# Kernel tuning notes

Measured on AMD Instinct MI355X. Metric: run time of the kernel, lower is better.

Reference implementation:

```python
import jax, jax.numpy as jnp
import numpy as np

NUM_HEADS = 8


def _conv1(x, w, b):
    # 1x1x1 Conv3d == per-voxel channel linear map. x: [B,C,D,H,W], w: [O,C], b: [O]
    return jnp.einsum('bcdhw,oc->bodhw', x, w) + b[None, :, None, None, None]


def setup_inputs() -> dict:
    key = jax.random.key(0)
    ks = jax.random.split(key, 7)
    B, C, D, H, W = 1, 64, 16, 16, 16
    s = 0.02
    return {
        'decoder_features': jax.random.normal(ks[0], (B, C, D, H, W), jnp.float32),
        'mae_features': jax.random.normal(ks[1], (B, C, D, H, W), jnp.float32),
        'q_w': jax.random.normal(ks[2], (C, C), jnp.float32) * s,
        'q_b': jnp.zeros((C,), jnp.float32),
        'k_w': jax.random.normal(ks[3], (C, C), jnp.float32) * s,
        'k_b': jnp.zeros((C,), jnp.float32),
        'v_w': jax.random.normal(ks[4], (C, C), jnp.float32) * s,
        'v_b': jnp.zeros((C,), jnp.float32),
        'o_w': jax.random.normal(ks[5], (C, C), jnp.float32) * s,
        'o_b': jnp.zeros((C,), jnp.float32),
    }


def reference(decoder_features, mae_features, q_w, q_b, k_w, k_b, v_w, v_b, o_w, o_b):
    B, C, D, H, W = decoder_features.shape
    nh = NUM_HEADS
    hd = C // nh
    N = D * H * W
    scale = hd ** -0.5

    def split_heads(x):
        # [B,C,D,H,W] -> [B, nh, N, hd]
        return x.reshape(B, nh, hd, N).transpose(0, 1, 3, 2)

    Q = split_heads(_conv1(decoder_features, q_w, q_b))
    K = split_heads(_conv1(mae_features, k_w, k_b))
    V = split_heads(_conv1(mae_features, v_w, v_b))

    attn = jax.nn.softmax(jnp.einsum('bhnc,bhmc->bhnm', Q, K) * scale, axis=-1)
    out = jnp.einsum('bhnm,bhmc->bhnc', attn, V)  # [B, nh, N, hd]
    out = out.transpose(0, 1, 3, 2).reshape(B, C, D, H, W)
    return _conv1(out, o_w, o_b)
```

## Files before the change

kernel.cpp:

```cpp
#include <hip/hip_runtime.h>
#include <hip/hip_bf16.h>
#include <math.h>


#define N_VOX 4096
#define NH 8
#define KS 8
#define KPS (N_VOX / KS)
#define QSCALE 0.51010813f

typedef unsigned short ushort_t;
typedef __attribute__((ext_vector_type(8))) short bf16x8;
typedef __attribute__((ext_vector_type(16))) float f32x16;

__device__ __forceinline__ unsigned short f2bf(float f) {
  union { float f; unsigned u; } v; v.f = f;
  unsigned r = v.u + 0x7FFFu + ((v.u >> 16) & 1u);
  return (unsigned short)(r >> 16);
}
__device__ __forceinline__ unsigned pk2bf(float a, float b) {
  __hip_bfloat162 h = __float22bfloat162_rn(float2{a, b});
  union { __hip_bfloat162 h; unsigned u; } c; c.h = h;
  return c.u;
}
__device__ __forceinline__ float ex2(float x) { return __builtin_amdgcn_exp2f(x); }

__global__ __launch_bounds__(256) void qkv_pack(
    const float* __restrict__ dec, const float* __restrict__ mae,
    const float* __restrict__ qw, const float* __restrict__ qb_,
    const float* __restrict__ kw, const float* __restrict__ kb,
    const float* __restrict__ vw, const float* __restrict__ vb,
    ushort_t* __restrict__ Qp, ushort_t* __restrict__ KpZ,
    ushort_t* __restrict__ VtP) {
  const int bx = blockIdx.x;
  const int n = blockIdx.y * 256 + threadIdx.x;

  if (bx < 8) {
    const int h = bx;
    float x[64];
#pragma unroll
    for (int c = 0; c < 64; ++c) x[c] = dec[c * N_VOX + n];
    float qv[8];
#pragma unroll
    for (int j = 0; j < 8; ++j) {
      const int o = h * 8 + j;
      float a = qb_[o];
#pragma unroll
      for (int c = 0; c < 64; ++c) a = fmaf(x[c], qw[o * 64 + c], a);
      qv[j] = a * QSCALE;
    }
    uint4 pk;
    pk.x = pk2bf(qv[0], qv[1]); pk.y = pk2bf(qv[2], qv[3]);
    pk.z = pk2bf(qv[4], qv[5]); pk.w = pk2bf(qv[6], qv[7]);
    *(uint4*)(Qp + ((size_t)h * N_VOX + n) * 8) = pk;
  } else {
    const int h = bx - 8;
    float x[64];
#pragma unroll
    for (int c = 0; c < 64; ++c) x[c] = mae[c * N_VOX + n];
    float kv[8], vv[8];
#pragma unroll
    for (int j = 0; j < 8; ++j) {
      const int o = h * 8 + j;
      float a = kb[o], v = vb[o];
#pragma unroll
      for (int c = 0; c < 64; ++c) {
        a = fmaf(x[c], kw[o * 64 + c], a);
        v = fmaf(x[c], vw[o * 64 + c], v);
      }
      kv[j] = a; vv[j] = v;
    }
    uint4 pk;
    pk.x = pk2bf(kv[0], kv[1]); pk.y = pk2bf(kv[2], kv[3]);
    pk.z = pk2bf(kv[4], kv[5]); pk.w = pk2bf(kv[6], kv[7]);
    ushort_t* krow = KpZ + ((size_t)h * N_VOX + n) * 16;
    *(uint4*)(krow) = pk;
    *(uint4*)(krow + 8) = make_uint4(0, 0, 0, 0);

    const size_t base =
        (((size_t)h * (N_VOX / 16) + (n >> 4)) * 64 + ((n >> 3) & 1) * 32) * 8 +
        (n & 7);
#pragma unroll
    for (int d = 0; d < 8; ++d) VtP[base + (size_t)d * 8] = f2bf(vv[d]);
    VtP[base + 8 * 8] = 0x3F80;
  }
}

__global__ __launch_bounds__(256, 4) void attn_mfma(
    const ushort_t* __restrict__ Qp, const ushort_t* __restrict__ KpZ,
    const ushort_t* __restrict__ VtP, float* __restrict__ o_part) {
  const int tid = threadIdx.x;
  const int lane = tid & 63;
  const int wave = tid >> 6;
  const int l31 = lane & 31;
  const int lhalf = lane >> 5;
  const int h = blockIdx.y;
  const int ks = blockIdx.z;
  const int qb = blockIdx.x * 256 + wave * 64;

  __shared__ ushort_t P_lds[8][32 * 36];

  bf16x8 qfrag0 = *(const bf16x8*)(Qp + ((size_t)h * N_VOX + qb + l31) * 8);
  bf16x8 qfrag1 = *(const bf16x8*)(Qp + ((size_t)h * N_VOX + qb + 32 + l31) * 8);

  f32x16 zf, acc0, acc1;
#pragma unroll
  for (int i = 0; i < 16; ++i) { zf[i] = 0.f; acc0[i] = 0.f; acc1[i] = 0.f; }

  const ushort_t* KpH = KpZ + (size_t)h * N_VOX * 16 + lhalf * 8;
  const ushort_t* VtPH = VtP + (size_t)h * (N_VOX / 16) * 64 * 8;
  ushort_t* pb0 = &P_lds[wave * 2 + 0][l31 * 36];
  ushort_t* pb1 = &P_lds[wave * 2 + 1][l31 * 36];
  const int kbeg = ks * KPS;

#pragma unroll 1
  for (int kk = 0; kk < KPS; kk += 32) {
    const int kcur = kbeg + kk;
    bf16x8 kf = *(const bf16x8*)(KpH + (size_t)(kcur + l31) * 16);
    bf16x8 vf0 = *(const bf16x8*)(VtPH + ((size_t)((kcur >> 4) + 0) * 64 + lane) * 8);
    bf16x8 vf1 = *(const bf16x8*)(VtPH + ((size_t)((kcur >> 4) + 1) * 64 + lane) * 8);

    f32x16 s0 = __builtin_amdgcn_mfma_f32_32x32x16_bf16(kf, qfrag0, zf, 0, 0, 0);
    f32x16 s1 = __builtin_amdgcn_mfma_f32_32x32x16_bf16(kf, qfrag1, zf, 0, 0, 0);

#pragma unroll
    for (int G = 0; G < 4; ++G) {
      uint2 w;
      w.x = pk2bf(ex2(s0[G * 4 + 0]), ex2(s0[G * 4 + 1]));
      w.y = pk2bf(ex2(s0[G * 4 + 2]), ex2(s0[G * 4 + 3]));
      *(uint2*)(pb0 + G * 8 + lhalf * 4) = w;
    }
#pragma unroll
    for (int G = 0; G < 4; ++G) {
      uint2 w;
      w.x = pk2bf(ex2(s1[G * 4 + 0]), ex2(s1[G * 4 + 1]));
      w.y = pk2bf(ex2(s1[G * 4 + 2]), ex2(s1[G * 4 + 3]));
      *(uint2*)(pb1 + G * 8 + lhalf * 4) = w;
    }

#pragma unroll
    for (int grp = 0; grp < 2; ++grp) {
      union { bf16x8 v; uint2 u[2]; } p0, p1;
      p0.u[0] = *(const uint2*)(pb0 + grp * 16 + lhalf * 8);
      p0.u[1] = *(const uint2*)(pb0 + grp * 16 + lhalf * 8 + 4);
      p1.u[0] = *(const uint2*)(pb1 + grp * 16 + lhalf * 8);
      p1.u[1] = *(const uint2*)(pb1 + grp * 16 + lhalf * 8 + 4);
      const bf16x8 vf = grp ? vf1 : vf0;
      acc0 = __builtin_amdgcn_mfma_f32_32x32x16_bf16(p0.v, vf, acc0, 0, 0, 0);
      acc1 = __builtin_amdgcn_mfma_f32_32x32x16_bf16(p1.v, vf, acc1, 0, 0, 0);
    }
  }

  if (l31 < 9) {
    float* ob = o_part + ((size_t)(ks * NH + h) * 9 + l31) * N_VOX;
#pragma unroll
    for (int t = 0; t < 2; ++t) {
      const f32x16 a = t ? acc1 : acc0;
      const int qst = qb + t * 32 + 4 * lhalf;
#pragma unroll
      for (int G = 0; G < 4; ++G) {
        float4 v4 = make_float4(a[G * 4 + 0], a[G * 4 + 1], a[G * 4 + 2], a[G * 4 + 3]);
        *(float4*)(ob + qst + 8 * G) = v4;
      }
    }
  }
}

__global__ __launch_bounds__(256) void combine_proj(
    const float* __restrict__ o_part, const float* __restrict__ ow,
    const float* __restrict__ obias, float* __restrict__ out) {
  const int og = blockIdx.x;
  const int n = blockIdx.y * 256 + threadIdx.x;

  float rinv[NH];
#pragma unroll
  for (int h = 0; h < NH; ++h) {
    float l = 0.f;
#pragma unroll
    for (int s = 0; s < KS; ++s)
      l += o_part[((size_t)(s * NH + h) * 9 + 8) * N_VOX + n];
    rinv[h] = 1.0f / l;
  }

  float acc[8];
#pragma unroll
  for (int j = 0; j < 8; ++j) acc[j] = obias[og * 8 + j];

#pragma unroll 2
  for (int c = 0; c < 64; ++c) {
    const int h = c >> 3, d = c & 7;
    float so = 0.f;
#pragma unroll
    for (int s = 0; s < KS; ++s)
      so += o_part[((size_t)(s * NH + h) * 9 + d) * N_VOX + n];
    const float x = so * rinv[h];
#pragma unroll
    for (int j = 0; j < 8; ++j)
      acc[j] = fmaf(x, ow[(og * 8 + j) * 64 + c], acc[j]);
  }
#pragma unroll
  for (int j = 0; j < 8; ++j) out[(size_t)(og * 8 + j) * N_VOX + n] = acc[j];
}

extern "C" void kernel_launch(void* const* d_in, const int* in_sizes, int n_in,
                              void* d_out, int out_size, void* d_ws, size_t ws_size,
                              hipStream_t stream) {
  const float* dec = (const float*)d_in[0];
  const float* mae = (const float*)d_in[1];
  const float* qw = (const float*)d_in[2];
  const float* qb = (const float*)d_in[3];
  const float* kw = (const float*)d_in[4];
  const float* kb = (const float*)d_in[5];
  const float* vw = (const float*)d_in[6];
  const float* vb = (const float*)d_in[7];
  const float* ow = (const float*)d_in[8];
  const float* ob = (const float*)d_in[9];
  float* out = (float*)d_out;
  char* ws = (char*)d_ws;

  const size_t OFF_QP = 0;
  const size_t OFF_KP = 0x80000;
  const size_t OFF_VT = 0x180000;
  const size_t OFF_OPART = 0x380000;

  ushort_t* Qp = (ushort_t*)(ws + OFF_QP);
  ushort_t* KpZ = (ushort_t*)(ws + OFF_KP);
  ushort_t* VtP = (ushort_t*)(ws + OFF_VT);
  float* o_part = (float*)(ws + OFF_OPART);

  qkv_pack<<<dim3(16, 16), 256, 0, stream>>>(dec, mae, qw, qb, kw, kb, vw, vb,
                                             Qp, KpZ, VtP);
  attn_mfma<<<dim3(16, 8, KS), 256, 0, stream>>>(Qp, KpZ, VtP, o_part);
  combine_proj<<<dim3(8, 16), 256, 0, stream>>>(o_part, ow, ob, out);
}
```

Before: 154.9 us.

## Fuse QKV, attention, and projection into one persistent kernel with grid barriers

Replaces the three kernel launches with a single 1024-block kernel that runs the QKV projection, split-K attention, and combine/output projection as phases separated by a software grid barrier built on atomics. The goal is to remove launch overhead and the gaps between kernels. The combine phase is reworked to give each block 4 output channels instead of 8 across 256 blocks. The barrier needs all 1024 blocks resident at once, which means 4 blocks per CU of 256 threads; if occupancy falls short it deadlocks. It also adds a memset launch and idles blocks during the light phases.

Result: slower. 376.6 us (+143.1%).

```diff
diff --git a/kernel.cpp b/kernel.cpp
--- a/kernel.cpp
+++ b/kernel.cpp
@@ -7,6 +7,7 @@
 #define NH 8
 #define KS 8
 #define KPS (N_VOX / KS)
+#define NBLK 1024
 #define QSCALE 0.51010813f
 
 typedef unsigned short ushort_t;
@@ -25,181 +26,208 @@
 }
 __device__ __forceinline__ float ex2(float x) { return __builtin_amdgcn_exp2f(x); }
 
-__global__ __launch_bounds__(256) void qkv_pack(
+__device__ __forceinline__ void grid_barrier(unsigned* cnt, unsigned* gen,
+                                             int tid) {
+  __syncthreads();
+  if (tid == 0) {
+    __threadfence();
+    unsigned g = atomicAdd(gen, 0u);
+    unsigned v = atomicAdd(cnt, 1u);
+    if (v == NBLK - 1) {
+      atomicExch(cnt, 0u);
+      __threadfence();
+      atomicAdd(gen, 1u);
+    } else {
+      while (atomicAdd(gen, 0u) == g) __builtin_amdgcn_s_sleep(4);
+    }
+    __threadfence();
+  }
+  __syncthreads();
+}
+
+__global__ __launch_bounds__(256, 4) void fused_xattn(
     const float* __restrict__ dec, const float* __restrict__ mae,
     const float* __restrict__ qw, const float* __restrict__ qb_,
     const float* __restrict__ kw, const float* __restrict__ kb,
     const float* __restrict__ vw, const float* __restrict__ vb,
+    const float* __restrict__ ow, const float* __restrict__ obias,
     ushort_t* __restrict__ Qp, ushort_t* __restrict__ KpZ,
-    ushort_t* __restrict__ VtP) {
-  const int bx = blockIdx.x;
-  const int n = blockIdx.y * 256 + threadIdx.x;
-
-  if (bx < 8) {
-    const int h = bx;
-    float x[64];
-#pragma unroll
-    for (int c = 0; c < 64; ++c) x[c] = dec[c * N_VOX + n];
-    float qv[8];
-#pragma unroll
-    for (int j = 0; j < 8; ++j) {
-      const int o = h * 8 + j;
-      float a = qb_[o];
-#pragma unroll
-      for (int c = 0; c < 64; ++c) a = fmaf(x[c], qw[o * 64 + c], a);
-      qv[j] = a * QSCALE;
-    }
-    uint4 pk;
-    pk.x = pk2bf(qv[0], qv[1]); pk.y = pk2bf(qv[2], qv[3]);
-    pk.z = pk2bf(qv[4], qv[5]); pk.w = pk2bf(qv[6], qv[7]);
-    *(uint4*)(Qp + ((size_t)h * N_VOX + n) * 8) = pk;
-  } else {
-    const int h = bx - 8;
-    float x[64];
-#pragma unroll
-    for (int c = 0; c < 64; ++c) x[c] = mae[c * N_VOX + n];
-    float kv[8], vv[8];
-#pragma unroll
-    for (int j = 0; j < 8; ++j) {
-      const int o = h * 8 + j;
-      float a = kb[o], v = vb[o];
-#pragma unroll
-      for (int c = 0; c < 64; ++c) {
-        a = fmaf(x[c], kw[o * 64 + c], a);
-        v = fmaf(x[c], vw[o * 64 + c], v);
-      }
-      kv[j] = a; vv[j] = v;
-    }
-    uint4 pk;
-    pk.x = pk2bf(kv[0], kv[1]); pk.y = pk2bf(kv[2], kv[3]);
-    pk.z = pk2bf(kv[4], kv[5]); pk.w = pk2bf(kv[6], kv[7]);
-    ushort_t* krow = KpZ + ((size_t)h * N_VOX + n) * 16;
-    *(uint4*)(krow) = pk;
-    *(uint4*)(krow + 8) = make_uint4(0, 0, 0, 0);
-
-    const size_t base =
-        (((size_t)h * (N_VOX / 16) + (n >> 4)) * 64 + ((n >> 3) & 1) * 32) * 8 +
-        (n & 7);
-#pragma unroll
-    for (int d = 0; d < 8; ++d) VtP[base + (size_t)d * 8] = f2bf(vv[d]);
-    VtP[base + 8 * 8] = 0x3F80;
-  }
-}
-
-__global__ __launch_bounds__(256, 4) void attn_mfma(
-    const ushort_t* __restrict__ Qp, const ushort_t* __restrict__ KpZ,
-    const ushort_t* __restrict__ VtP, float* __restrict__ o_part) {
+    ushort_t* __restrict__ VtP, float* __restrict__ o_part,
+    unsigned* __restrict__ bar, float* __restrict__ out) {
+  const int b = blockIdx.x;
   const int tid = threadIdx.x;
-  const int lane = tid & 63;
-  const int wave = tid >> 6;
-  const int l31 = lane & 31;
-  const int lhalf = lane >> 5;
-  const int h = blockIdx.y;
-  const int ks = blockIdx.z;
-  const int qb = blockIdx.x * 256 + wave * 64;
+  unsigned* cnt = bar;
+  unsigned* gen = bar + 1;
 
   __shared__ ushort_t P_lds[8][32 * 36];
 
-  bf16x8 qfrag0 = *(const bf16x8*)(Qp + ((size_t)h * N_VOX + qb + l31) * 8);
-  bf16x8 qfrag1 = *(const bf16x8*)(Qp + ((size_t)h * N_VOX + qb + 32 + l31) * 8);
-
-  f32x16 zf, acc0, acc1;
-#pragma unroll
-  for (int i = 0; i < 16; ++i) { zf[i] = 0.f; acc0[i] = 0.f; acc1[i] = 0.f; }
-
-  const ushort_t* KpH = KpZ + (size_t)h * N_VOX * 16 + lhalf * 8;
-  const ushort_t* VtPH = VtP + (size_t)h * (N_VOX / 16) * 64 * 8;
-  ushort_t* pb0 = &P_lds[wave * 2 + 0][l31 * 36];
-  ushort_t* pb1 = &P_lds[wave * 2 + 1][l31 * 36];
-  const int kbeg = ks * KPS;
+  if (b < 256) {
+    const int bx = b >> 4;
+    const int n = (b & 15) * 256 + tid;
+    if (bx < 8) {
+      const int h = bx;
+      float x[64];
+#pragma unroll
+      for (int c = 0; c < 64; ++c) x[c] = dec[c * N_VOX + n];
+      float qv[8];
+#pragma unroll
+      for (int j = 0; j < 8; ++j) {
+        const int o = h * 8 + j;
+        float a = qb_[o];
+#pragma unroll
+        for (int c = 0; c < 64; ++c) a = fmaf(x[c], qw[o * 64 + c], a);
+        qv[j] = a * QSCALE;
+      }
+      uint4 pk;
+      pk.x = pk2bf(qv[0], qv[1]); pk.y = pk2bf(qv[2], qv[3]);
+      pk.z = pk2bf(qv[4], qv[5]); pk.w = pk2bf(qv[6], qv[7]);
+      *(uint4*)(Qp + ((size_t)h * N_VOX + n) * 8) = pk;
+    } else {
+      const int h = bx - 8;
+      float x[64];
+#pragma unroll
+      for (int c = 0; c < 64; ++c) x[c] = mae[c * N_VOX + n];
+      float kv[8], vv[8];
+#pragma unroll
+      for (int j = 0; j < 8; ++j) {
+        const int o = h * 8 + j;
+        float a = kb[o], v = vb[o];
+#pragma unroll
+        for (int c = 0; c < 64; ++c) {
+          a = fmaf(x[c], kw[o * 64 + c], a);
+          v = fmaf(x[c], vw[o * 64 + c], v);
+        }
+        kv[j] = a; vv[j] = v;
+      }
+      uint4 pk;
+      pk.x = pk2bf(kv[0], kv[1]); pk.y = pk2bf(kv[2], kv[3]);
+      pk.z = pk2bf(kv[4], kv[5]); pk.w = pk2bf(kv[6], kv[7]);
+      ushort_t* krow = KpZ + ((size_t)h * N_VOX + n) * 16;
+      *(uint4*)(krow) = pk;
+      *(uint4*)(krow + 8) = make_uint4(0, 0, 0, 0);
+
+      const size_t base =
+          (((size_t)h * (N_VOX / 16) + (n >> 4)) * 64 + ((n >> 3) & 1) * 32) * 8 +
+          (n & 7);
+#pragma unroll
+      for (int d = 0; d < 8; ++d) VtP[base + (size_t)d * 8] = f2bf(vv[d]);
+      VtP[base + 8 * 8] = 0x3F80;
+    }
+  }
+
+  grid_barrier(cnt, gen, tid);
+
+  {
+    const int lane = tid & 63;
+    const int wave = tid >> 6;
+    const int l31 = lane & 31;
+    const int lhalf = lane >> 5;
+    const int qt = b & 15;
+    const int h = (b >> 4) & 7;
+    const int ks = b >> 7;
+    const int qb = qt * 256 + wave * 64;
+
+    bf16x8 qfrag0 = *(const bf16x8*)(Qp + ((size_t)h * N_VOX + qb + l31) * 8);
+    bf16x8 qfrag1 = *(const bf16x8*)(Qp + ((size_t)h * N_VOX + qb + 32 + l31) * 8);
+
+    f32x16 zf, acc0, acc1;
+#pragma unroll
+    for (int i = 0; i < 16; ++i) { zf[i] = 0.f; acc0[i] = 0.f; acc1[i] = 0.f; }
+
+    const ushort_t* KpH = KpZ + (size_t)h * N_VOX * 16 + lhalf * 8;
+    const ushort_t* VtPH = VtP + (size_t)h * (N_VOX / 16) * 64 * 8;
+    ushort_t* pb0 = &P_lds[wave * 2 + 0][l31 * 36];
+    ushort_t* pb1 = &P_lds[wave * 2 + 1][l31 * 36];
+    const int kbeg = ks * KPS;
 
 #pragma unroll 1
-  for (int kk = 0; kk < KPS; kk += 32) {
-    const int kcur = kbeg + kk;
-    bf16x8 kf = *(const bf16x8*)(KpH + (size_t)(kcur + l31) * 16);
-    bf16x8 vf0 = *(const bf16x8*)(VtPH + ((size_t)((kcur >> 4) + 0) * 64 + lane) * 8);
-    bf16x8 vf1 = *(const bf16x8*)(VtPH + ((size_t)((kcur >> 4) + 1) * 64 + lane) * 8);
-
-    f32x16 s0 = __builtin_amdgcn_mfma_f32_32x32x16_bf16(kf, qfrag0, zf, 0, 0, 0);
-    f32x16 s1 = __builtin_amdgcn_mfma_f32_32x32x16_bf16(kf, qfrag1, zf, 0, 0, 0);
-
-#pragma unroll
-    for (int G = 0; G < 4; ++G) {
-      uint2 w;
-      w.x = pk2bf(ex2(s0[G * 4 + 0]), ex2(s0[G * 4 + 1]));
-      w.y = pk2bf(ex2(s0[G * 4 + 2]), ex2(s0[G * 4 + 3]));
-      *(uint2*)(pb0 + G * 8 + lhalf * 4) = w;
-    }
-#pragma unroll
-    for (int G = 0; G < 4; ++G) {
-      uint2 w;
-      w.x = pk2bf(ex2(s1[G * 4 + 0]), ex2(s1[G * 4 + 1]));
-      w.y = pk2bf(ex2(s1[G * 4 + 2]), ex2(s1[G * 4 + 3]));
-      *(uint2*)(pb1 + G * 8 + lhalf * 4) = w;
-    }
-
-#pragma unroll
-    for (int grp = 0; grp < 2; ++grp) {
-      union { bf16x8 v; uint2 u[2]; } p0, p1;
-      p0.u[0] = *(const uint2*)(pb0 + grp * 16 + lhalf * 8);
-      p0.u[1] = *(const uint2*)(pb0 + grp * 16 + lhalf * 8 + 4);
-      p1.u[0] = *(const uint2*)(pb1 + grp * 16 + lhalf * 8);
-      p1.u[1] = *(const uint2*)(pb1 + grp * 16 + lhalf * 8 + 4);
-      const bf16x8 vf = grp ? vf1 : vf0;
-      acc0 = __builtin_amdgcn_mfma_f32_32x32x16_bf16(p0.v, vf, acc0, 0, 0, 0);
-      acc1 = __builtin_amdgcn_mfma_f32_32x32x16_bf16(p1.v, vf, acc1, 0, 0, 0);
-    }
-  }
-
-  if (l31 < 9) {
-    float* ob = o_part + ((size_t)(ks * NH + h) * 9 + l31) * N_VOX;
-#pragma unroll
-    for (int t = 0; t < 2; ++t) {
-      const f32x16 a = t ? acc1 : acc0;
-      const int qst = qb + t * 32 + 4 * lhalf;
+    for (int kk = 0; kk < KPS; kk += 32) {
+      const int kcur = kbeg + kk;
+      bf16x8 kf = *(const bf16x8*)(KpH + (size_t)(kcur + l31) * 16);
+      bf16x8 vf0 = *(const bf16x8*)(VtPH + ((size_t)((kcur >> 4) + 0) * 64 + lane) * 8);
+      bf16x8 vf1 = *(const bf16x8*)(VtPH + ((size_t)((kcur >> 4) + 1) * 64 + lane) * 8);
+
+      f32x16 s0 = __builtin_amdgcn_mfma_f32_32x32x16_bf16(kf, qfrag0, zf, 0, 0, 0);
+      f32x16 s1 = __builtin_amdgcn_mfma_f32_32x32x16_bf16(kf, qfrag1, zf, 0, 0, 0);
+
 #pragma unroll
       for (int G = 0; G < 4; ++G) {
-        float4 v4 = make_float4(a[G * 4 + 0], a[G * 4 + 1], a[G * 4 + 2], a[G * 4 + 3]);
-        *(float4*)(ob + qst + 8 * G) = v4;
-      }
-    }
-  }
-}
-
-__global__ __launch_bounds__(256) void combine_proj(
-    const float* __restrict__ o_part, const float* __restrict__ ow,
-    const float* __restrict__ obias, float* __restrict__ out) {
-  const int og = blockIdx.x;
-  const int n = blockIdx.y * 256 + threadIdx.x;
-
-  float rinv[NH];
-#pragma unroll
-  for (int h = 0; h < NH; ++h) {
-    float l = 0.f;
-#pragma unroll
-    for (int s = 0; s < KS; ++s)
-      l += o_part[((size_t)(s * NH + h) * 9 + 8) * N_VOX + n];
-    rinv[h] = 1.0f / l;
-  }
-
-  float acc[8];
-#pragma unroll
-  for (int j = 0; j < 8; ++j) acc[j] = obias[og * 8 + j];
+        uint2 w;
+        w.x = pk2bf(ex2(s0[G * 4 + 0]), ex2(s0[G * 4 + 1]));
+        w.y = pk2bf(ex2(s0[G * 4 + 2]), ex2(s0[G * 4 + 3]));
+        *(uint2*)(pb0 + G * 8 + lhalf * 4) = w;
+      }
+#pragma unroll
+      for (int G = 0; G < 4; ++G) {
+        uint2 w;
+        w.x = pk2bf(ex2(s1[G * 4 + 0]), ex2(s1[G * 4 + 1]));
+        w.y = pk2bf(ex2(s1[G * 4 + 2]), ex2(s1[G * 4 + 3]));
+        *(uint2*)(pb1 + G * 8 + lhalf * 4) = w;
+      }
+
+#pragma unroll
+      for (int grp = 0; grp < 2; ++grp) {
+        union { bf16x8 v; uint2 u[2]; } p0, p1;
+        p0.u[0] = *(const uint2*)(pb0 + grp * 16 + lhalf * 8);
+        p0.u[1] = *(const uint2*)(pb0 + grp * 16 + lhalf * 8 + 4);
+        p1.u[0] = *(const uint2*)(pb1 + grp * 16 + lhalf * 8);
+        p1.u[1] = *(const uint2*)(pb1 + grp * 16 + lhalf * 8 + 4);
+        const bf16x8 vf = grp ? vf1 : vf0;
+        acc0 = __builtin_amdgcn_mfma_f32_32x32x16_bf16(p0.v, vf, acc0, 0, 0, 0);
+        acc1 = __builtin_amdgcn_mfma_f32_32x32x16_bf16(p1.v, vf, acc1, 0, 0, 0);
+      }
+    }
+
+    if (l31 < 9) {
+      float* ob = o_part + ((size_t)(ks * NH + h) * 9 + l31) * N_VOX;
+#pragma unroll
+      for (int t = 0; t < 2; ++t) {
+        const f32x16 a = t ? acc1 : acc0;
+        const int qst = qb + t * 32 + 4 * lhalf;
+#pragma unroll
+        for (int G = 0; G < 4; ++G) {
+          float4 v4 = make_float4(a[G * 4 + 0], a[G * 4 + 1], a[G * 4 + 2], a[G * 4 + 3]);
+          *(float4*)(ob + qst + 8 * G) = v4;
+        }
+      }
+    }
+  }
+
+  grid_barrier(cnt, gen, tid);
+
+  if (b < 256) {
+    const int og = b >> 4;
+    const int n = (b & 15) * 256 + tid;
+
+    float rinv[NH];
+#pragma unroll
+    for (int h = 0; h < NH; ++h) {
+      float l = 0.f;
+#pragma unroll
+      for (int s = 0; s < KS; ++s)
+        l += o_part[((size_t)(s * NH + h) * 9 + 8) * N_VOX + n];
+      rinv[h] = 1.0f / l;
+    }
+
+    float acc[4];
+#pragma unroll
+    for (int j = 0; j < 4; ++j) acc[j] = obias[og * 4 + j];
 
 #pragma unroll 2
-  for (int c = 0; c < 64; ++c) {
-    const int h = c >> 3, d = c & 7;
-    float so = 0.f;
-#pragma unroll
-    for (int s = 0; s < KS; ++s)
-      so += o_part[((size_t)(s * NH + h) * 9 + d) * N_VOX + n];
-    const float x = so * rinv[h];
-#pragma unroll
-    for (int j = 0; j < 8; ++j)
-      acc[j] = fmaf(x, ow[(og * 8 + j) * 64 + c], acc[j]);
-  }
-#pragma unroll
-  for (int j = 0; j < 8; ++j) out[(size_t)(og * 8 + j) * N_VOX + n] = acc[j];
+    for (int c = 0; c < 64; ++c) {
+      const int h = c >> 3, d = c & 7;
+      float so = 0.f;
+#pragma unroll
+      for (int s = 0; s < KS; ++s)
+        so += o_part[((size_t)(s * NH + h) * 9 + d) * N_VOX + n];
+      const float x = so * rinv[h];
+#pragma unroll
+      for (int j = 0; j < 4; ++j)
+        acc[j] = fmaf(x, ow[(og * 4 + j) * 64 + c], acc[j]);
+    }
+#pragma unroll
+    for (int j = 0; j < 4; ++j) out[(size_t)(og * 4 + j) * N_VOX + n] = acc[j];
+  }
 }
 
 extern "C" void kernel_launch(void* const* d_in, const int* in_sizes, int n_in,
@@ -222,14 +250,17 @@
   const size_t OFF_KP = 0x80000;
   const size_t OFF_VT = 0x180000;
   const size_t OFF_OPART = 0x380000;
+  const size_t OFF_BAR = OFF_OPART + (size_t)KS * NH * 9 * N_VOX * 4;
 
   ushort_t* Qp = (ushort_t*)(ws + OFF_QP);
   ushort_t* KpZ = (ushort_t*)(ws + OFF_KP);
   ushort_t* VtP = (ushort_t*)(ws + OFF_VT);
   float* o_part = (float*)(ws + OFF_OPART);
-
-  qkv_pack<<<dim3(16, 16), 256, 0, stream>>>(dec, mae, qw, qb, kw, kb, vw, vb,
-                                             Qp, KpZ, VtP);
-  attn_mfma<<<dim3(16, 8, KS), 256, 0, stream>>>(Qp, KpZ, VtP, o_part);
-  combine_proj<<<dim3(8, 16), 256, 0, stream>>>(o_part, ow, ob, out);
-}
+  unsigned* bar = (unsigned*)(ws + OFF_BAR);
+
+  hipMemsetAsync(bar, 0, 2 * sizeof(unsigned), stream);
+
+  fused_xattn<<<dim3(NBLK), dim3(256), 0, stream>>>(
+      dec, mae, qw, qb, kw, kb, vw, vb, ow, ob,
+      Qp, KpZ, VtP, o_part, bar, out);
+}
```

## Halve per-wave query tile in attention and split combine from output projection

Applied to the files above, without the earlier changes.

Each attention wave now handles 32 queries instead of 64, so the grid doubles and the occupancy hint rises to 8 blocks per CU. The aim is more parallelism and latency hiding. The cost is that every K/V fragment is loaded twice as often relative to the MFMA work it feeds. The old combine_proj kernel is split into an elementwise combine kernel that writes a normalized buffer, followed by a separate output projection. That split adds one kernel launch and an extra round trip through global memory, in exchange for simpler per-thread work and fewer redundant o_part reads.

Result: faster. 133.4 us (-13.9%).

```diff
diff --git a/kernel.cpp b/kernel.cpp
--- a/kernel.cpp
+++ b/kernel.cpp
@@ -86,7 +86,7 @@
   }
 }
 
-__global__ __launch_bounds__(256, 4) void attn_mfma(
+__global__ __launch_bounds__(256, 8) void attn_mfma(
     const ushort_t* __restrict__ Qp, const ushort_t* __restrict__ KpZ,
     const ushort_t* __restrict__ VtP, float* __restrict__ o_part) {
   const int tid = threadIdx.x;
@@ -96,21 +96,22 @@
   const int lhalf = lane >> 5;
   const int h = blockIdx.y;
   const int ks = blockIdx.z;
-  const int qb = blockIdx.x * 256 + wave * 64;
-
-  __shared__ ushort_t P_lds[8][32 * 36];
-
-  bf16x8 qfrag0 = *(const bf16x8*)(Qp + ((size_t)h * N_VOX + qb + l31) * 8);
-  bf16x8 qfrag1 = *(const bf16x8*)(Qp + ((size_t)h * N_VOX + qb + 32 + l31) * 8);
-
-  f32x16 zf, acc0, acc1;
-#pragma unroll
-  for (int i = 0; i < 16; ++i) { zf[i] = 0.f; acc0[i] = 0.f; acc1[i] = 0.f; }
+  const int qb = blockIdx.x * 128 + wave * 32;
+
+  __shared__ ushort_t P_lds[4][32 * 36];
+
+  bf16x8 qfrag = *(const bf16x8*)(Qp + ((size_t)h * N_VOX + qb + l31) * 8);
+
+  f32x16 acc;
+#pragma unroll
+  for (int i = 0; i < 16; ++i) acc[i] = 0.f;
+  f32x16 zf;
+#pragma unroll
+  for (int i = 0; i < 16; ++i) zf[i] = 0.f;
 
   const ushort_t* KpH = KpZ + (size_t)h * N_VOX * 16 + lhalf * 8;
   const ushort_t* VtPH = VtP + (size_t)h * (N_VOX / 16) * 64 * 8;
-  ushort_t* pb0 = &P_lds[wave * 2 + 0][l31 * 36];
-  ushort_t* pb1 = &P_lds[wave * 2 + 1][l31 * 36];
+  ushort_t* pb = &P_lds[wave][l31 * 36];
   const int kbeg = ks * KPS;
 
 #pragma unroll 1
@@ -120,86 +121,69 @@
     bf16x8 vf0 = *(const bf16x8*)(VtPH + ((size_t)((kcur >> 4) + 0) * 64 + lane) * 8);
     bf16x8 vf1 = *(const bf16x8*)(VtPH + ((size_t)((kcur >> 4) + 1) * 64 + lane) * 8);
 
-    f32x16 s0 = __builtin_amdgcn_mfma_f32_32x32x16_bf16(kf, qfrag0, zf, 0, 0, 0);
-    f32x16 s1 = __builtin_amdgcn_mfma_f32_32x32x16_bf16(kf, qfrag1, zf, 0, 0, 0);
+    f32x16 s = __builtin_amdgcn_mfma_f32_32x32x16_bf16(kf, qfrag, zf, 0, 0, 0);
 
 #pragma unroll
     for (int G = 0; G < 4; ++G) {
       uint2 w;
-      w.x = pk2bf(ex2(s0[G * 4 + 0]), ex2(s0[G * 4 + 1]));
-      w.y = pk2bf(ex2(s0[G * 4 + 2]), ex2(s0[G * 4 + 3]));
-      *(uint2*)(pb0 + G * 8 + lhalf * 4) = w;
-    }
-#pragma unroll
-    for (int G = 0; G < 4; ++G) {
-      uint2 w;
-      w.x = pk2bf(ex2(s1[G * 4 + 0]), ex2(s1[G * 4 + 1]));
-      w.y = pk2bf(ex2(s1[G * 4 + 2]), ex2(s1[G * 4 + 3]));
-      *(uint2*)(pb1 + G * 8 + lhalf * 4) = w;
+      w.x = pk2bf(ex2(s[G * 4 + 0]), ex2(s[G * 4 + 1]));
+      w.y = pk2bf(ex2(s[G * 4 + 2]), ex2(s[G * 4 + 3]));
+      *(uint2*)(pb + G * 8 + lhalf * 4) = w;
     }
 
 #pragma unroll
     for (int grp = 0; grp < 2; ++grp) {
-      union { bf16x8 v; uint2 u[2]; } p0, p1;
-      p0.u[0] = *(const uint2*)(pb0 + grp * 16 + lhalf * 8);
-      p0.u[1] = *(const uint2*)(pb0 + grp * 16 + lhalf * 8 + 4);
-      p1.u[0] = *(const uint2*)(pb1 + grp * 16 + lhalf * 8);
-      p1.u[1] = *(const uint2*)(pb1 + grp * 16 + lhalf * 8 + 4);
-      const bf16x8 vf = grp ? vf1 : vf0;
-      acc0 = __builtin_amdgcn_mfma_f32_32x32x16_bf16(p0.v, vf, acc0, 0, 0, 0);
-      acc1 = __builtin_amdgcn_mfma_f32_32x32x16_bf16(p1.v, vf, acc1, 0, 0, 0);
+      union { bf16x8 v; uint2 u[2]; } p;
+      p.u[0] = *(const uint2*)(pb + grp * 16 + lhalf * 8);
+      p.u[1] = *(const uint2*)(pb + grp * 16 + lhalf * 8 + 4);
+      acc = __builtin_amdgcn_mfma_f32_32x32x16_bf16(p.v, grp ? vf1 : vf0, acc,
+                                                    0, 0, 0);
     }
   }
 
   if (l31 < 9) {
     float* ob = o_part + ((size_t)(ks * NH + h) * 9 + l31) * N_VOX;
-#pragma unroll
-    for (int t = 0; t < 2; ++t) {
-      const f32x16 a = t ? acc1 : acc0;
-      const int qst = qb + t * 32 + 4 * lhalf;
-#pragma unroll
-      for (int G = 0; G < 4; ++G) {
-        float4 v4 = make_float4(a[G * 4 + 0], a[G * 4 + 1], a[G * 4 + 2], a[G * 4 + 3]);
-        *(float4*)(ob + qst + 8 * G) = v4;
-      }
-    }
-  }
-}
-
-__global__ __launch_bounds__(256) void combine_proj(
-    const float* __restrict__ o_part, const float* __restrict__ ow,
+    const int qst = qb + 4 * lhalf;
+#pragma unroll
+    for (int G = 0; G < 4; ++G) {
+      float4 v4 = make_float4(acc[G * 4 + 0], acc[G * 4 + 1], acc[G * 4 + 2],
+                              acc[G * 4 + 3]);
+      *(float4*)(ob + qst + 8 * G) = v4;
+    }
+  }
+}
+
+__global__ __launch_bounds__(256) void combine(
+    const float* __restrict__ o_part, float* __restrict__ ocomb) {
+  const int t = blockIdx.x * 256 + threadIdx.x;
+  const int c = t >> 12, n = t & (N_VOX - 1);
+  const int h = c >> 3, d = c & 7;
+  float so = 0.f, sl = 0.f;
+#pragma unroll
+  for (int s = 0; s < KS; ++s) {
+    const float* base = o_part + ((size_t)(s * NH + h) * 9) * N_VOX;
+    so += base[d * N_VOX + n];
+    sl += base[8 * N_VOX + n];
+  }
+  ocomb[(size_t)c * N_VOX + n] = so / sl;
+}
+
+__global__ __launch_bounds__(256) void out_proj(
+    const float* __restrict__ ocomb, const float* __restrict__ ow,
     const float* __restrict__ obias, float* __restrict__ out) {
   const int og = blockIdx.x;
   const int n = blockIdx.y * 256 + threadIdx.x;
-
-  float rinv[NH];
-#pragma unroll
-  for (int h = 0; h < NH; ++h) {
-    float l = 0.f;
-#pragma unroll
-    for (int s = 0; s < KS; ++s)
-      l += o_part[((size_t)(s * NH + h) * 9 + 8) * N_VOX + n];
-    rinv[h] = 1.0f / l;
-  }
-
-  float acc[8];
-#pragma unroll
-  for (int j = 0; j < 8; ++j) acc[j] = obias[og * 8 + j];
-
-#pragma unroll 2
-  for (int c = 0; c < 64; ++c) {
-    const int h = c >> 3, d = c & 7;
-    float so = 0.f;
-#pragma unroll
-    for (int s = 0; s < KS; ++s)
-      so += o_part[((size_t)(s * NH + h) * 9 + d) * N_VOX + n];
-    const float x = so * rinv[h];
-#pragma unroll
-    for (int j = 0; j < 8; ++j)
-      acc[j] = fmaf(x, ow[(og * 8 + j) * 64 + c], acc[j]);
-  }
-#pragma unroll
-  for (int j = 0; j < 8; ++j) out[(size_t)(og * 8 + j) * N_VOX + n] = acc[j];
+  float x[64];
+#pragma unroll
+  for (int c = 0; c < 64; ++c) x[c] = ocomb[c * N_VOX + n];
+#pragma unroll
+  for (int j = 0; j < 8; ++j) {
+    const int o = og * 8 + j;
+    float acc = obias[o];
+#pragma unroll
+    for (int c = 0; c < 64; ++c) acc = fmaf(x[c], ow[o * 64 + c], acc);
+    out[o * N_VOX + n] = acc;
+  }
 }
 
 extern "C" void kernel_launch(void* const* d_in, const int* in_sizes, int n_in,
@@ -222,14 +206,17 @@
   const size_t OFF_KP = 0x80000;
   const size_t OFF_VT = 0x180000;
   const size_t OFF_OPART = 0x380000;
+  const size_t OFF_OCOMB = OFF_OPART + (size_t)KS * NH * 9 * N_VOX * 4;
 
   ushort_t* Qp = (ushort_t*)(ws + OFF_QP);
   ushort_t* KpZ = (ushort_t*)(ws + OFF_KP);
   ushort_t* VtP = (ushort_t*)(ws + OFF_VT);
   float* o_part = (float*)(ws + OFF_OPART);
+  float* ocomb = (float*)(ws + OFF_OCOMB);
 
   qkv_pack<<<dim3(16, 16), 256, 0, stream>>>(dec, mae, qw, qb, kw, kb, vw, vb,
                                              Qp, KpZ, VtP);
-  attn_mfma<<<dim3(16, 8, KS), 256, 0, stream>>>(Qp, KpZ, VtP, o_part);
-  combine_proj<<<dim3(8, 16), 256, 0, stream>>>(o_part, ow, ob, out);
-}
+  attn_mfma<<<dim3(32, 8, KS), 256, 0, stream>>>(Qp, KpZ, VtP, o_part);
+  combine<<<1024, 256, 0, stream>>>(o_part, ocomb);
+  out_proj<<<dim3(8, 16), 256, 0, stream>>>(ocomb, ow, ob, out);
+}
```
